# Kernel tuning notes

Hardware: AMD Instinct MI355X
Metric: run time of the kernel (lower is better)

Reference implementation:

```python
import jax, jax.numpy as jnp
import numpy as np

EPS = 1e-7  # keras.backend.epsilon()


def setup_inputs() -> dict:
    key = jax.random.key(0)
    kx, kw, ku = jax.random.split(key, 3)
    B, S, F = 16, 4096, 512
    x = jax.random.normal(kx, (B, S, F), dtype=jnp.float32)
    # glorot-uniform-scaled weights
    limW = np.sqrt(6.0 / (F + F)).astype(np.float32)
    W = jax.random.uniform(kw, (F, F), dtype=jnp.float32, minval=-limW, maxval=limW)
    b = jnp.zeros((F,), dtype=jnp.float32)
    limu = np.sqrt(6.0 / (F + 1)).astype(np.float32)
    u = jax.random.uniform(ku, (F,), dtype=jnp.float32, minval=-limu, maxval=limu)
    return {"x": x, "W": W, "b": b, "u": u}


def reference(x, W, b, u):
    # x: [B,S,F]  W: [F,F]  b: [F]  u: [F]
    h = jnp.tanh(jnp.einsum('bsf,fg->bsg', x, W) + b)   # [B,S,F]
    scores = jnp.einsum('bsf,f->bs', h, u)              # [B,S]
    e = jnp.exp(scores)
    # NOTE: faithful to the source, normalization is GLOBAL over all B*S scores
    a = e / (jnp.sum(e) + EPS)                          # [B,S]
    out = jnp.einsum('bsf,bs->bf', x, a)                # [B,F] weighted-sum pool over steps
    return out
```

## Files before the change

### kernel.cpp

```cpp
#include <hip/hip_runtime.h>
#include <stdint.h>

#define EPSV 1e-7f
#define FDIM 512
#define ROWS 128
#define BK 32
#define PCOLS 256
#define NROWS 65536

typedef __bf16 bf16_t;
typedef bf16_t bf16x8 __attribute__((ext_vector_type(8)));
typedef unsigned short ushort8 __attribute__((ext_vector_type(8)));
typedef float f32x4 __attribute__((ext_vector_type(4)));

#define AS1 __attribute__((address_space(1)))
#define AS3 __attribute__((address_space(3)))

__device__ __forceinline__ unsigned short f2bf(float f) {
  union { float f; unsigned int u; } c; c.f = f;
  unsigned int u = c.u;
  unsigned int r = u + 0x7fffu + ((u >> 16) & 1u);
  return (unsigned short)(r >> 16);
}
__device__ __forceinline__ float bf2f(unsigned short s) {
  union { unsigned int u; float f; } c; c.u = ((unsigned int)s) << 16;
  return c.f;
}

__device__ __forceinline__ float fast_tanh(float x) {
  x = fminf(15.0f, fmaxf(-15.0f, x));
  float t = __expf(2.0f * x);
  return 1.0f - 2.0f * __builtin_amdgcn_rcpf(t + 1.0f);
}

__global__ void convert_W(const float* __restrict__ W, unsigned short* __restrict__ Wt,
                          float* __restrict__ sumE) {
  if (blockIdx.x == 0 && threadIdx.x == 0) *sumE = 0.0f;
  __shared__ unsigned short tile[32][34];
  const int t = threadIdx.x;
  const int tx = t & 31, ty = t >> 5;
  const int bn = blockIdx.x & 15, bk = blockIdx.x >> 4;
  const int k0 = bk * 32, n0 = bn * 32;
#pragma unroll
  for (int i = 0; i < 4; ++i) {
    int r = ty + i * 8;
    tile[r][tx] = f2bf(W[(size_t)(k0 + r) * FDIM + n0 + tx]);
  }
  __syncthreads();
#pragma unroll
  for (int i = 0; i < 4; ++i) {
    int r = ty + i * 8;
    Wt[(size_t)(n0 + r) * FDIM + k0 + tx] = tile[tx][r];
  }
}

#define ISSUE_B(buf_, pass_, kc_)                                              \
  do {                                                                         \
    _Pragma("unroll") for (int i_ = 0; i_ < 2; ++i_) {                         \
      const int rb_ = (w * 2 + i_) * 16;                                       \
      const int rl_ = rb_ + (lane >> 2);                                       \
      const int j_ = (lane & 3) ^ ((rl_ >> 2) & 3);                            \
      const unsigned short* g_ =                                               \
          Wt + (size_t)((pass_) * PCOLS + rl_) * FDIM + (kc_) * BK + j_ * 8;   \
      unsigned short* l_ = (unsigned short*)(&sB[buf_][0] + rb_ * BK);         \
      __builtin_amdgcn_global_load_lds((AS1 void*)(g_), (AS3 void*)(l_), 16,   \
                                       0, 0);                                  \
    }                                                                          \
  } while (0)

__global__ __launch_bounds__(512, 2) void fused_score_pool(
    const float* __restrict__ x, const unsigned short* __restrict__ Wt,
    const float* __restrict__ bvec, const float* __restrict__ uvec,
    float* __restrict__ ppool, float* __restrict__ sumE) {
  __shared__ alignas(16) unsigned short sA[ROWS * FDIM];
  __shared__ alignas(16) unsigned short sB[2][PCOLS * BK];

  const int t = threadIdx.x;
  const int lane = t & 63;
  const int w = t >> 6;
  const int wm = w & 1;
  const int wn = w >> 1;
  const int quad = lane >> 4;
  const int l15 = lane & 15;
  const int m0 = blockIdx.x * ROWS;

  ISSUE_B(0, 0, 0);

#pragma unroll
  for (int p = 0; p < 16; ++p) {
    const int row = p * 8 + w;
    const float* g = x + (size_t)(m0 + row) * FDIM + lane * 8;
    float4 lo = *(const float4*)g;
    float4 hi = *(const float4*)(g + 4);
    ushort8 v;
    v[0] = f2bf(lo.x); v[1] = f2bf(lo.y); v[2] = f2bf(lo.z); v[3] = f2bf(lo.w);
    v[4] = f2bf(hi.x); v[5] = f2bf(hi.y); v[6] = f2bf(hi.z); v[7] = f2bf(hi.w);
    const int jp = lane ^ (row & 7);
    *(ushort8*)(void*)(sA + row * FDIM + jp * 8) = v;
  }
  __syncthreads();

  float sc[4][4];
#pragma unroll
  for (int mi = 0; mi < 4; ++mi)
#pragma unroll
    for (int r = 0; r < 4; ++r) sc[mi][r] = 0.0f;

  int cur = 0;
  for (int pass = 0; pass < 2; ++pass) {
    f32x4 acc[4][4];
#pragma unroll
    for (int mi = 0; mi < 4; ++mi)
#pragma unroll
      for (int ni = 0; ni < 4; ++ni) acc[mi][ni] = (f32x4){0.f, 0.f, 0.f, 0.f};

#pragma unroll 2
    for (int kc = 0; kc < 16; ++kc) {
      const int s = pass * 16 + kc + 1;
      if (s < 32) ISSUE_B(cur ^ 1, (s >> 4), (s & 15));

      bf16x8 bfr[4], af[4];
#pragma unroll
      for (int ni = 0; ni < 4; ++ni) {
        const int r = wn * 64 + ni * 16 + l15;
        const int phys = quad ^ ((r >> 2) & 3);
        bfr[ni] = *(const bf16x8*)(const void*)(&sB[cur][0] + r * BK + phys * 8);
      }
#pragma unroll
      for (int mi = 0; mi < 4; ++mi) {
        const int row = wm * 64 + mi * 16 + l15;
        const int g = kc * 4 + quad;
        const int phys = g ^ (row & 7);
        af[mi] = *(const bf16x8*)(const void*)(sA + row * FDIM + phys * 8);
      }

#pragma unroll
      for (int mi = 0; mi < 4; ++mi)
#pragma unroll
        for (int ni = 0; ni < 4; ++ni)
          acc[mi][ni] = __builtin_amdgcn_mfma_f32_16x16x32_bf16(
              af[mi], bfr[ni], acc[mi][ni], 0, 0, 0);

      __syncthreads();
      cur ^= 1;
    }

#pragma unroll
    for (int ni = 0; ni < 4; ++ni) {
      const int cl = pass * PCOLS + wn * 64 + ni * 16 + l15;
      const float uu = uvec[cl], bb = bvec[cl];
#pragma unroll
      for (int mi = 0; mi < 4; ++mi)
#pragma unroll
        for (int r = 0; r < 4; ++r)
          sc[mi][r] += uu * fast_tanh(acc[mi][ni][r] + bb);
    }
  }

  float* sBf = (float*)&sB[0][0];
  float* red = sBf;
  float* score_s = sBf + 4096;
  float* e_s = sBf + 4096 + 128;

  if (t < ROWS) score_s[t] = 0.0f;
  __syncthreads();

#pragma unroll
  for (int mi = 0; mi < 4; ++mi)
#pragma unroll
    for (int r = 0; r < 4; ++r) {
      float v = sc[mi][r];
      v += __shfl_xor(v, 1); v += __shfl_xor(v, 2);
      v += __shfl_xor(v, 4); v += __shfl_xor(v, 8);
      if (l15 == 0)
        atomicAdd(&score_s[wm * 64 + mi * 16 + quad * 4 + r], v);
    }
  __syncthreads();

  if (t < ROWS) {
    const float e = __expf(score_s[t]);
    e_s[t] = e;
    float v = e;
    v += __shfl_xor(v, 1);  v += __shfl_xor(v, 2);  v += __shfl_xor(v, 4);
    v += __shfl_xor(v, 8);  v += __shfl_xor(v, 16); v += __shfl_xor(v, 32);
    if (lane == 0) atomicAdd(sumE, v);
  }
  __syncthreads();

  float a[8];
#pragma unroll
  for (int jj = 0; jj < 8; ++jj) a[jj] = 0.0f;
#pragma unroll
  for (int rr = 0; rr < 16; ++rr) {
    const int row = w * 16 + rr;
    const int jp = lane ^ (row & 7);
    const ushort8 v = *(const ushort8*)(const void*)(sA + row * FDIM + jp * 8);
    const float wg = e_s[row];
#pragma unroll
    for (int jj = 0; jj < 8; ++jj) a[jj] += bf2f(v[jj]) * wg;
  }
  *(float4*)&red[w * FDIM + lane * 8]     = (float4){a[0], a[1], a[2], a[3]};
  *(float4*)&red[w * FDIM + lane * 8 + 4] = (float4){a[4], a[5], a[6], a[7]};
  __syncthreads();
  {
    float sv = 0.0f;
#pragma unroll
    for (int g = 0; g < 8; ++g) sv += red[g * FDIM + t];
    ppool[(size_t)blockIdx.x * FDIM + t] = sv;
  }
}

__global__ __launch_bounds__(256) void finalize(
    const float* __restrict__ ppool, const float* __restrict__ sumE,
    float* __restrict__ out) {
  const int i = blockIdx.x * 256 + threadIdx.x;
  const int b = i >> 9, f = i & 511;
  const float* p = ppool + (size_t)b * 32 * FDIM + f;
  float s = 0.0f;
#pragma unroll
  for (int c = 0; c < 32; ++c) s += p[(size_t)c * FDIM];
  out[i] = s / (*sumE + EPSV);
}

extern "C" void kernel_launch(void* const* d_in, const int* in_sizes, int n_in,
                              void* d_out, int out_size, void* d_ws, size_t ws_size,
                              hipStream_t stream) {
  (void)in_sizes; (void)n_in; (void)out_size; (void)ws_size;
  const float* x = (const float*)d_in[0];
  const float* W = (const float*)d_in[1];
  const float* b = (const float*)d_in[2];
  const float* u = (const float*)d_in[3];
  float* out = (float*)d_out;

  char* p = (char*)d_ws;
  unsigned short* Wt = (unsigned short*)p;  p += (size_t)FDIM * FDIM * 2;
  float* sumE = (float*)p;                  p += 256;
  float* ppool = (float*)p;                 p += (size_t)(NROWS / ROWS) * FDIM * 4;

  convert_W<<<dim3(256), dim3(256), 0, stream>>>(W, Wt, sumE);
  fused_score_pool<<<dim3(NROWS / ROWS), dim3(512), 0, stream>>>(
      x, Wt, b, u, ppool, sumE);
  finalize<<<dim3(32), dim3(256), 0, stream>>>(ppool, sumE, out);
}
```

Baseline: 248.8 us.

## Halve row tile, read W fragments directly from global, drop LDS staging of W

The fused kernel now processes 64 rows per block instead of 128. Each of the 8 waves owns 64 output columns across all rows, so the two-pass loop, the double-buffered LDS staging of W and the per-iteration barriers are gone. W is pre-laid out in k-chunked form so MFMA B fragments load straight from global/L2, and LDS use drops so occupancy can rise to 4 blocks per CU. The pooling step becomes a per-column loop over rows without the cross-wave reduction buffer. Finalize sums twice as many partials. The risk is that each block re-reads the whole W from cache with no LDS reuse, and the per-thread pooling does strided scalar LDS reads.

```diff
diff --git a/kernel.cpp b/kernel.cpp
--- a/kernel.cpp
+++ b/kernel.cpp
@@ -3,18 +3,14 @@
 
 #define EPSV 1e-7f
 #define FDIM 512
-#define ROWS 128
-#define BK 32
-#define PCOLS 256
+#define ROWS 64
 #define NROWS 65536
+#define NBLK (NROWS / ROWS)
 
 typedef __bf16 bf16_t;
 typedef bf16_t bf16x8 __attribute__((ext_vector_type(8)));
 typedef unsigned short ushort8 __attribute__((ext_vector_type(8)));
 typedef float f32x4 __attribute__((ext_vector_type(4)));
-
-#define AS1 __attribute__((address_space(1)))
-#define AS3 __attribute__((address_space(3)))
 
 __device__ __forceinline__ unsigned short f2bf(float f) {
   union { float f; unsigned int u; } c; c.f = f;
@@ -33,7 +29,7 @@
   return 1.0f - 2.0f * __builtin_amdgcn_rcpf(t + 1.0f);
 }
 
-__global__ void convert_W(const float* __restrict__ W, unsigned short* __restrict__ Wt,
+__global__ void convert_W(const float* __restrict__ W, unsigned short* __restrict__ Wt2,
                           float* __restrict__ sumE) {
   if (blockIdx.x == 0 && threadIdx.x == 0) *sumE = 0.0f;
   __shared__ unsigned short tile[32][34];
@@ -50,44 +46,29 @@
 #pragma unroll
   for (int i = 0; i < 4; ++i) {
     int r = ty + i * 8;
-    Wt[(size_t)(n0 + r) * FDIM + k0 + tx] = tile[tx][r];
+    Wt2[(size_t)(k0 >> 5) * (FDIM * 32) + (size_t)(n0 + r) * 32 + tx] = tile[tx][r];
   }
 }
 
-#define ISSUE_B(buf_, pass_, kc_)                                              \
-  do {                                                                         \
-    _Pragma("unroll") for (int i_ = 0; i_ < 2; ++i_) {                         \
-      const int rb_ = (w * 2 + i_) * 16;                                       \
-      const int rl_ = rb_ + (lane >> 2);                                       \
-      const int j_ = (lane & 3) ^ ((rl_ >> 2) & 3);                            \
-      const unsigned short* g_ =                                               \
-          Wt + (size_t)((pass_) * PCOLS + rl_) * FDIM + (kc_) * BK + j_ * 8;   \
-      unsigned short* l_ = (unsigned short*)(&sB[buf_][0] + rb_ * BK);         \
-      __builtin_amdgcn_global_load_lds((AS1 void*)(g_), (AS3 void*)(l_), 16,   \
-                                       0, 0);                                  \
-    }                                                                          \
-  } while (0)
-
-__global__ __launch_bounds__(512, 2) void fused_score_pool(
-    const float* __restrict__ x, const unsigned short* __restrict__ Wt,
+__global__ __launch_bounds__(512, 4) void fused_score_pool(
+    const float* __restrict__ x, const unsigned short* __restrict__ Wt2,
     const float* __restrict__ bvec, const float* __restrict__ uvec,
     float* __restrict__ ppool, float* __restrict__ sumE) {
   __shared__ alignas(16) unsigned short sA[ROWS * FDIM];
-  __shared__ alignas(16) unsigned short sB[2][PCOLS * BK];
+  __shared__ float score_s[ROWS];
+  __shared__ float e_s[ROWS];
 
   const int t = threadIdx.x;
   const int lane = t & 63;
   const int w = t >> 6;
-  const int wm = w & 1;
-  const int wn = w >> 1;
   const int quad = lane >> 4;
   const int l15 = lane & 15;
   const int m0 = blockIdx.x * ROWS;
 
-  ISSUE_B(0, 0, 0);
+  if (t < ROWS) score_s[t] = 0.0f;
 
 #pragma unroll
-  for (int p = 0; p < 16; ++p) {
+  for (int p = 0; p < 8; ++p) {
     const int row = p * 8 + w;
     const float* g = x + (size_t)(m0 + row) * FDIM + lane * 8;
     float4 lo = *(const float4*)g;
@@ -100,80 +81,55 @@
   }
   __syncthreads();
 
-  float sc[4][4];
+  f32x4 acc[4][4];
 #pragma unroll
   for (int mi = 0; mi < 4; ++mi)
 #pragma unroll
-    for (int r = 0; r < 4; ++r) sc[mi][r] = 0.0f;
+    for (int ni = 0; ni < 4; ++ni) acc[mi][ni] = (f32x4){0.f, 0.f, 0.f, 0.f};
 
-  int cur = 0;
-  for (int pass = 0; pass < 2; ++pass) {
-    f32x4 acc[4][4];
+  const unsigned short* bp = Wt2 + (size_t)(w * 64 + l15) * 32 + quad * 8;
+
+#pragma unroll 2
+  for (int kc = 0; kc < 16; ++kc) {
+    bf16x8 bfr[4], af[4];
+#pragma unroll
+    for (int ni = 0; ni < 4; ++ni)
+      bfr[ni] = *(const bf16x8*)(const void*)(bp + (size_t)kc * (FDIM * 32) + ni * 512);
+#pragma unroll
+    for (int mi = 0; mi < 4; ++mi) {
+      const int row = mi * 16 + l15;
+      const int phys = (kc * 4 + quad) ^ (row & 7);
+      af[mi] = *(const bf16x8*)(const void*)(sA + row * FDIM + phys * 8);
+    }
+    __builtin_amdgcn_s_setprio(1);
 #pragma unroll
     for (int mi = 0; mi < 4; ++mi)
 #pragma unroll
-      for (int ni = 0; ni < 4; ++ni) acc[mi][ni] = (f32x4){0.f, 0.f, 0.f, 0.f};
-
-#pragma unroll 2
-    for (int kc = 0; kc < 16; ++kc) {
-      const int s = pass * 16 + kc + 1;
-      if (s < 32) ISSUE_B(cur ^ 1, (s >> 4), (s & 15));
-
-      bf16x8 bfr[4], af[4];
-#pragma unroll
-      for (int ni = 0; ni < 4; ++ni) {
-        const int r = wn * 64 + ni * 16 + l15;
-        const int phys = quad ^ ((r >> 2) & 3);
-        bfr[ni] = *(const bf16x8*)(const void*)(&sB[cur][0] + r * BK + phys * 8);
-      }
-#pragma unroll
-      for (int mi = 0; mi < 4; ++mi) {
-        const int row = wm * 64 + mi * 16 + l15;
-        const int g = kc * 4 + quad;
-        const int phys = g ^ (row & 7);
-        af[mi] = *(const bf16x8*)(const void*)(sA + row * FDIM + phys * 8);
-      }
-
-#pragma unroll
-      for (int mi = 0; mi < 4; ++mi)
-#pragma unroll
-        for (int ni = 0; ni < 4; ++ni)
-          acc[mi][ni] = __builtin_amdgcn_mfma_f32_16x16x32_bf16(
-              af[mi], bfr[ni], acc[mi][ni], 0, 0, 0);
-
-      __syncthreads();
-      cur ^= 1;
-    }
-
-#pragma unroll
-    for (int ni = 0; ni < 4; ++ni) {
-      const int cl = pass * PCOLS + wn * 64 + ni * 16 + l15;
-      const float uu = uvec[cl], bb = bvec[cl];
-#pragma unroll
-      for (int mi = 0; mi < 4; ++mi)
-#pragma unroll
-        for (int r = 0; r < 4; ++r)
-          sc[mi][r] += uu * fast_tanh(acc[mi][ni][r] + bb);
-    }
+      for (int ni = 0; ni < 4; ++ni)
+        acc[mi][ni] = __builtin_amdgcn_mfma_f32_16x16x32_bf16(
+            af[mi], bfr[ni], acc[mi][ni], 0, 0, 0);
+    __builtin_amdgcn_s_setprio(0);
   }
 
-  float* sBf = (float*)&sB[0][0];
-  float* red = sBf;
-  float* score_s = sBf + 4096;
-  float* e_s = sBf + 4096 + 128;
-
-  if (t < ROWS) score_s[t] = 0.0f;
-  __syncthreads();
-
+  float uu[4], bb[4];
+#pragma unroll
+  for (int ni = 0; ni < 4; ++ni) {
+    const int cl = w * 64 + ni * 16 + l15;
+    uu[ni] = uvec[cl];
+    bb[ni] = bvec[cl];
+  }
 #pragma unroll
   for (int mi = 0; mi < 4; ++mi)
 #pragma unroll
     for (int r = 0; r < 4; ++r) {
-      float v = sc[mi][r];
+      float v = 0.0f;
+#pragma unroll
+      for (int ni = 0; ni < 4; ++ni)
+        v += uu[ni] * fast_tanh(acc[mi][ni][r] + bb[ni]);
       v += __shfl_xor(v, 1); v += __shfl_xor(v, 2);
       v += __shfl_xor(v, 4); v += __shfl_xor(v, 8);
       if (l15 == 0)
-        atomicAdd(&score_s[wm * 64 + mi * 16 + quad * 4 + r], v);
+        atomicAdd(&score_s[mi * 16 + quad * 4 + r], v);
     }
   __syncthreads();
 
@@ -187,26 +143,16 @@
   }
   __syncthreads();
 
-  float a[8];
-#pragma unroll
-  for (int jj = 0; jj < 8; ++jj) a[jj] = 0.0f;
-#pragma unroll
-  for (int rr = 0; rr < 16; ++rr) {
-    const int row = w * 16 + rr;
-    const int jp = lane ^ (row & 7);
-    const ushort8 v = *(const ushort8*)(const void*)(sA + row * FDIM + jp * 8);
-    const float wg = e_s[row];
-#pragma unroll
-    for (int jj = 0; jj < 8; ++jj) a[jj] += bf2f(v[jj]) * wg;
-  }
-  *(float4*)&red[w * FDIM + lane * 8]     = (float4){a[0], a[1], a[2], a[3]};
-  *(float4*)&red[w * FDIM + lane * 8 + 4] = (float4){a[4], a[5], a[6], a[7]};
-  __syncthreads();
   {
-    float sv = 0.0f;
-#pragma unroll
-    for (int g = 0; g < 8; ++g) sv += red[g * FDIM + t];
-    ppool[(size_t)blockIdx.x * FDIM + t] = sv;
+    const int col = t;
+    const int jblk = col >> 3, jj = col & 7;
+    float s = 0.0f;
+#pragma unroll 8
+    for (int row = 0; row < ROWS; ++row) {
+      const int phys = ((jblk ^ (row & 7)) << 3) + jj;
+      s += bf2f(sA[row * FDIM + phys]) * e_s[row];
+    }
+    ppool[(size_t)blockIdx.x * FDIM + col] = s;
   }
 }
 
@@ -215,10 +161,10 @@
     float* __restrict__ out) {
   const int i = blockIdx.x * 256 + threadIdx.x;
   const int b = i >> 9, f = i & 511;
-  const float* p = ppool + (size_t)b * 32 * FDIM + f;
+  const float* p = ppool + (size_t)b * 64 * FDIM + f;
   float s = 0.0f;
 #pragma unroll
-  for (int c = 0; c < 32; ++c) s += p[(size_t)c * FDIM];
+  for (int c = 0; c < 64; ++c) s += p[(size_t)c * FDIM];
   out[i] = s / (*sumE + EPSV);
 }
 
@@ -233,12 +179,12 @@
   float* out = (float*)d_out;
 
   char* p = (char*)d_ws;
-  unsigned short* Wt = (unsigned short*)p;  p += (size_t)FDIM * FDIM * 2;
-  float* sumE = (float*)p;                  p += 256;
-  float* ppool = (float*)p;                 p += (size_t)(NROWS / ROWS) * FDIM * 4;
+  unsigned short* Wt2 = (unsigned short*)p;  p += (size_t)FDIM * FDIM * 2;
+  float* sumE = (float*)p;                   p += 256;
+  float* ppool = (float*)p;                  p += (size_t)NBLK * FDIM * 4;
 
-  convert_W<<<dim3(256), dim3(256), 0, stream>>>(W, Wt, sumE);
-  fused_score_pool<<<dim3(NROWS / ROWS), dim3(512), 0, stream>>>(
-      x, Wt, b, u, ppool, sumE);
+  convert_W<<<dim3(256), dim3(256), 0, stream>>>(W, Wt2, sumE);
+  fused_score_pool<<<dim3(NBLK), dim3(512), 0, stream>>>(
+      x, Wt2, b, u, ppool, sumE);
   finalize<<<dim3(32), dim3(256), 0, stream>>>(ppool, sumE, out);
 }
```

Measured after the change: 236.5 us. 1.05x faster.
